# Performance work log

Hardware: AMD Instinct MI355X
Metric: run time of the kernel (lower is better)

The kernel has to match this reference:

```python
import jax, jax.numpy as jnp
import numpy as np

VOCAB = 100000
EMB_DIM = 64
NUM_DT_BUCKETS = 128
PAD_DT_ID = 0
B, L = 4096, 200


def setup_inputs() -> dict:
    key = jax.random.key(0)
    k1, k2, k3, k4, k5, k6 = jax.random.split(key, 6)
    items_pad = jax.random.randint(k1, (B, L), 0, VOCAB, dtype=jnp.int64 if jax.config.jax_enable_x64 else jnp.int32)
    dts_pad = jax.random.randint(k2, (B, L), 0, NUM_DT_BUCKETS, dtype=items_pad.dtype)
    mask = jax.random.randint(k3, (B, L), 0, 2) > 0
    mask = mask.at[:, 0].set(True)  # guarantee at least one valid position per row
    cand_items = jax.random.randint(k4, (B,), 0, VOCAB, dtype=items_pad.dtype)
    item_emb = jax.random.normal(k5, (VOCAB, EMB_DIM), dtype=jnp.float32) * 0.02
    dt_gate = jax.random.normal(k6, (NUM_DT_BUCKETS, 1), dtype=jnp.float32) * 0.02
    raw_tau = jnp.asarray(0.0, dtype=jnp.float32)
    return {
        "items_pad": items_pad,
        "dts_pad": dts_pad,
        "mask": mask,
        "cand_items": cand_items,
        "item_emb": item_emb,
        "dt_gate": dt_gate,
        "raw_tau": raw_tau,
    }


def reference(items_pad, dts_pad, mask, cand_items, item_emb, dt_gate, raw_tau):
    # padding_idx=0 on dt_gate: row PAD_DT_ID is zero
    dt_gate = dt_gate.at[PAD_DT_ID].set(0.0)
    k = item_emb[items_pad]                # [B, L, D]
    q = item_emb[cand_items]               # [B, D]
    sim = jnp.einsum('bld,bd->bl', k, q)   # [B, L]
    gate = dt_gate[dts_pad][..., 0]        # [B, L]
    tau = jax.nn.softplus(raw_tau) + 1e-6
    logits = sim * gate / tau
    logits = jnp.where(mask, logits, -jnp.inf)
    attn = jax.nn.softmax(logits, axis=1)  # [B, L]
    u = jnp.einsum('bl,bld->bd', attn, k)  # [B, D]
    return u, attn, tau
```

## Files before the change

### kernel.cpp

```cpp
#include <hip/hip_runtime.h>
#include <math.h>


constexpr int Bsz  = 4096;
constexpr int Lseq = 200;
constexpr int Dim  = 64;
constexpr int WPB  = 4;

__global__ __launch_bounds__(256, 2)
void cac_kernel(const int* __restrict__ items,
                const int* __restrict__ dts,
                const int* __restrict__ mask,
                const int* __restrict__ cand,
                const float* __restrict__ emb,
                const float* __restrict__ gate,
                const float* __restrict__ rawtau,
                float* __restrict__ out_u,
                float* __restrict__ out_attn,
                float* __restrict__ out_tau)
{
    __shared__ int   cpos[WPB][Lseq];
    __shared__ int   crow[WPB][Lseq];
    __shared__ float cgate[WPB][Lseq];
    __shared__ float clog[WPB][Lseq];

    const int tid  = threadIdx.x;
    const int wv   = tid >> 6;
    const int lane = tid & 63;
    const int b    = blockIdx.x * WPB + wv;

    const float raw = rawtau[0];
    const float sp  = (raw > 20.f) ? raw : log1pf(expf(raw));
    const float tau = sp + 1e-6f;
    const float inv_tau = 1.0f / tau;
    if (b == 0 && tid == 0) out_tau[0] = tau;

    int rowk[4], mk[4];
    float gk[4];
    #pragma unroll
    for (int k = 0; k < 4; ++k) {
        const int  p  = k * 64 + lane;
        const bool in = (p < Lseq);
        rowk[k] = in ? items[(size_t)b * Lseq + p] : 0;
        mk[k]   = in ? mask[(size_t)b * Lseq + p] : 0;
        const int dt = in ? dts[(size_t)b * Lseq + p] : 0;
        gk[k] = (dt == 0) ? 0.f : gate[dt];
    }

    unsigned long long bals[4];
    int offs[5];
    offs[0] = 0;
    #pragma unroll
    for (int k = 0; k < 4; ++k) {
        bals[k] = __ballot(mk[k] != 0);
        offs[k + 1] = offs[k] + __popcll(bals[k]);
    }
    const int cnt = offs[4];
    const unsigned long long ltmask = (1ull << lane) - 1ull;
    #pragma unroll
    for (int k = 0; k < 4; ++k) {
        if (mk[k]) {
            const int idx = offs[k] + __popcll(bals[k] & ltmask);
            cpos[wv][idx]  = k * 64 + lane;
            crow[wv][idx]  = rowk[k];
            cgate[wv][idx] = gk[k];
        }
    }

    const int r = lane >> 2;
    const int j = lane & 3;
    const float4* qrow = (const float4*)(emb + (size_t)cand[b] * Dim);
    float4 qv[4];
    #pragma unroll
    for (int i = 0; i < 4; ++i) qv[i] = qrow[i * 4 + j];

    float acc[16];
    #pragma unroll
    for (int i = 0; i < 16; ++i) acc[i] = 0.f;
    float m = -INFINITY, s_l = 0.f;

    const int ngrp = (cnt + 15) >> 4;
    for (int g = 0; g < ngrp; ++g) {
        const int  e     = g * 16 + r;
        const bool valid = (e < cnt);
        const int  ec    = valid ? e : (cnt - 1);
        const int  row   = crow[wv][ec];
        const float cg   = cgate[wv][ec];
        const float4* kp = (const float4*)(emb + (size_t)row * Dim);
        float4 kv[4];
        #pragma unroll
        for (int i = 0; i < 4; ++i) kv[i] = kp[i * 4 + j];

        float p = 0.f;
        #pragma unroll
        for (int i = 0; i < 4; ++i) {
            p = fmaf(kv[i].x, qv[i].x, p);
            p = fmaf(kv[i].y, qv[i].y, p);
            p = fmaf(kv[i].z, qv[i].z, p);
            p = fmaf(kv[i].w, qv[i].w, p);
        }
        p += __shfl_xor(p, 1, 64);
        p += __shfl_xor(p, 2, 64);

        const float logit = p * cg * inv_tau;
        const float leff  = valid ? logit : -INFINITY;

        float gm = leff;
        #pragma unroll
        for (int off = 4; off < 64; off <<= 1)
            gm = fmaxf(gm, __shfl_xor(gm, off, 64));

        if (gm > m) {
            const float scale = __expf(m - gm);
            s_l *= scale;
            #pragma unroll
            for (int i = 0; i < 16; ++i) acc[i] *= scale;
            m = gm;
        }

        const float wgt = __expf(leff - m);
        if (valid && j == 0) clog[wv][e] = logit;
        if (j == 0) s_l += wgt;
        #pragma unroll
        for (int i = 0; i < 4; ++i) {
            acc[4 * i + 0] = fmaf(wgt, kv[i].x, acc[4 * i + 0]);
            acc[4 * i + 1] = fmaf(wgt, kv[i].y, acc[4 * i + 1]);
            acc[4 * i + 2] = fmaf(wgt, kv[i].z, acc[4 * i + 2]);
            acc[4 * i + 3] = fmaf(wgt, kv[i].w, acc[4 * i + 3]);
        }
    }

    #pragma unroll
    for (int off = 4; off < 64; off <<= 1) {
        #pragma unroll
        for (int i = 0; i < 16; ++i) acc[i] += __shfl_xor(acc[i], off, 64);
    }
    float s = s_l;
    #pragma unroll
    for (int off = 1; off < 64; off <<= 1) s += __shfl_xor(s, off, 64);
    const float inv_s = 1.0f / s;

    if (r == 0) {
        float4* up = (float4*)(out_u + (size_t)b * Dim);
        #pragma unroll
        for (int i = 0; i < 4; ++i) {
            float4 o;
            o.x = acc[4 * i + 0] * inv_s;
            o.y = acc[4 * i + 1] * inv_s;
            o.z = acc[4 * i + 2] * inv_s;
            o.w = acc[4 * i + 3] * inv_s;
            up[i * 4 + j] = o;
        }
    }

    #pragma unroll
    for (int k = 0; k < 4; ++k) {
        const int p = k * 64 + lane;
        if (p < Lseq && !mk[k]) out_attn[(size_t)b * Lseq + p] = 0.f;
    }
    for (int e = lane; e < cnt; e += 64) {
        const float a = __expf(clog[wv][e] - m) * inv_s;
        out_attn[(size_t)b * Lseq + cpos[wv][e]] = a;
    }
}

extern "C" void kernel_launch(void* const* d_in, const int* in_sizes, int n_in,
                              void* d_out, int out_size, void* d_ws, size_t ws_size,
                              hipStream_t stream) {
    const int*   items  = (const int*)  d_in[0];
    const int*   dts    = (const int*)  d_in[1];
    const int*   mask   = (const int*)  d_in[2];
    const int*   cand   = (const int*)  d_in[3];
    const float* emb    = (const float*)d_in[4];
    const float* gate   = (const float*)d_in[5];
    const float* rawtau = (const float*)d_in[6];

    float* out_u    = (float*)d_out;
    float* out_attn = out_u + Bsz * Dim;
    float* out_tau  = out_attn + Bsz * Lseq;

    cac_kernel<<<Bsz / WPB, 256, 0, stream>>>(items, dts, mask, cand, emb, gate,
                                              rawtau, out_u, out_attn, out_tau);
}
```

Baseline: 100.8 us.

## Process two key rows per lane group and prefetch next group's embeddings

The online-softmax loop now handles 32 compacted positions per iteration, two per 4-lane group instead of one. It also software-prefetches the next iteration's embedding rows into registers before computing on the current ones. The aim is to raise memory-level parallelism on the random gather of embedding rows and to halve the number of cross-lane max reductions. In exchange register pressure roughly doubles for the key data (32 extra floats per lane), which could limit occupancy under the 256x2 launch bounds.

```diff
diff --git a/kernel.cpp b/kernel.cpp
--- a/kernel.cpp
+++ b/kernel.cpp
@@ -79,33 +79,61 @@
     for (int i = 0; i < 16; ++i) acc[i] = 0.f;
     float m = -INFINITY, s_l = 0.f;
 
-    const int ngrp = (cnt + 15) >> 4;
+    const int ngrp = (cnt + 31) >> 5;
+
+    int e0 = r, e1 = 16 + r;
+    int ec0 = (e0 < cnt) ? e0 : (cnt - 1);
+    int ec1 = (e1 < cnt) ? e1 : (cnt - 1);
+    int   row0 = crow[wv][ec0],  row1 = crow[wv][ec1];
+    float cg0  = cgate[wv][ec0], cg1  = cgate[wv][ec1];
+    float4 kv0[4], kv1[4];
+    {
+        const float4* kp0 = (const float4*)(emb + (size_t)row0 * Dim);
+        const float4* kp1 = (const float4*)(emb + (size_t)row1 * Dim);
+        #pragma unroll
+        for (int i = 0; i < 4; ++i) kv0[i] = kp0[i * 4 + j];
+        #pragma unroll
+        for (int i = 0; i < 4; ++i) kv1[i] = kp1[i * 4 + j];
+    }
+
     for (int g = 0; g < ngrp; ++g) {
-        const int  e     = g * 16 + r;
-        const bool valid = (e < cnt);
-        const int  ec    = valid ? e : (cnt - 1);
-        const int  row   = crow[wv][ec];
-        const float cg   = cgate[wv][ec];
-        const float4* kp = (const float4*)(emb + (size_t)row * Dim);
-        float4 kv[4];
-        #pragma unroll
-        for (int i = 0; i < 4; ++i) kv[i] = kp[i * 4 + j];
-
-        float p = 0.f;
+        const int gn = (g + 1 < ngrp) ? (g + 1) : g;
+        const int ne0 = gn * 32 + r, ne1 = ne0 + 16;
+        const int nec0 = (ne0 < cnt) ? ne0 : (cnt - 1);
+        const int nec1 = (ne1 < cnt) ? ne1 : (cnt - 1);
+        const int   nrow0 = crow[wv][nec0],  nrow1 = crow[wv][nec1];
+        const float ncg0  = cgate[wv][nec0], ncg1  = cgate[wv][nec1];
+        float4 nkv0[4], nkv1[4];
+        {
+            const float4* np0 = (const float4*)(emb + (size_t)nrow0 * Dim);
+            const float4* np1 = (const float4*)(emb + (size_t)nrow1 * Dim);
+            #pragma unroll
+            for (int i = 0; i < 4; ++i) nkv0[i] = np0[i * 4 + j];
+            #pragma unroll
+            for (int i = 0; i < 4; ++i) nkv1[i] = np1[i * 4 + j];
+        }
+
+        float p0 = 0.f, p1 = 0.f;
         #pragma unroll
         for (int i = 0; i < 4; ++i) {
-            p = fmaf(kv[i].x, qv[i].x, p);
-            p = fmaf(kv[i].y, qv[i].y, p);
-            p = fmaf(kv[i].z, qv[i].z, p);
-            p = fmaf(kv[i].w, qv[i].w, p);
-        }
-        p += __shfl_xor(p, 1, 64);
-        p += __shfl_xor(p, 2, 64);
-
-        const float logit = p * cg * inv_tau;
-        const float leff  = valid ? logit : -INFINITY;
-
-        float gm = leff;
+            p0 = fmaf(kv0[i].x, qv[i].x, p0);
+            p0 = fmaf(kv0[i].y, qv[i].y, p0);
+            p0 = fmaf(kv0[i].z, qv[i].z, p0);
+            p0 = fmaf(kv0[i].w, qv[i].w, p0);
+            p1 = fmaf(kv1[i].x, qv[i].x, p1);
+            p1 = fmaf(kv1[i].y, qv[i].y, p1);
+            p1 = fmaf(kv1[i].z, qv[i].z, p1);
+            p1 = fmaf(kv1[i].w, qv[i].w, p1);
+        }
+        p0 += __shfl_xor(p0, 1, 64);  p0 += __shfl_xor(p0, 2, 64);
+        p1 += __shfl_xor(p1, 1, 64);  p1 += __shfl_xor(p1, 2, 64);
+
+        const float logit0 = p0 * cg0 * inv_tau;
+        const float logit1 = p1 * cg1 * inv_tau;
+        const float leff0  = (e0 < cnt) ? logit0 : -INFINITY;
+        const float leff1  = (e1 < cnt) ? logit1 : -INFINITY;
+
+        float gm = fmaxf(leff0, leff1);
         #pragma unroll
         for (int off = 4; off < 64; off <<= 1)
             gm = fmaxf(gm, __shfl_xor(gm, off, 64));
@@ -118,16 +146,23 @@
             m = gm;
         }
 
-        const float wgt = __expf(leff - m);
-        if (valid && j == 0) clog[wv][e] = logit;
-        if (j == 0) s_l += wgt;
+        const float w0 = __expf(leff0 - m);
+        const float w1 = __expf(leff1 - m);
+        if (e0 < cnt && j == 0) clog[wv][e0] = logit0;
+        if (e1 < cnt && j == 0) clog[wv][e1] = logit1;
+        if (j == 0) s_l += w0 + w1;
         #pragma unroll
         for (int i = 0; i < 4; ++i) {
-            acc[4 * i + 0] = fmaf(wgt, kv[i].x, acc[4 * i + 0]);
-            acc[4 * i + 1] = fmaf(wgt, kv[i].y, acc[4 * i + 1]);
-            acc[4 * i + 2] = fmaf(wgt, kv[i].z, acc[4 * i + 2]);
-            acc[4 * i + 3] = fmaf(wgt, kv[i].w, acc[4 * i + 3]);
-        }
+            acc[4 * i + 0] = fmaf(w0, kv0[i].x, fmaf(w1, kv1[i].x, acc[4 * i + 0]));
+            acc[4 * i + 1] = fmaf(w0, kv0[i].y, fmaf(w1, kv1[i].y, acc[4 * i + 1]));
+            acc[4 * i + 2] = fmaf(w0, kv0[i].z, fmaf(w1, kv1[i].z, acc[4 * i + 2]));
+            acc[4 * i + 3] = fmaf(w0, kv0[i].w, fmaf(w1, kv1[i].w, acc[4 * i + 3]));
+        }
+
+        e0 = ne0; e1 = ne1;
+        cg0 = ncg0; cg1 = ncg1;
+        #pragma unroll
+        for (int i = 0; i < 4; ++i) { kv0[i] = nkv0[i]; kv1[i] = nkv1[i]; }
     }
 
     #pragma unroll
```

Result: no change. 102.6 us (+1.8%).

## Split each row across two wavefronts with shared-memory softmax merge

Applied to the files above, without the earlier changes.

Each batch row is now processed by two wavefronts instead of one. Each wavefront covers half of the compacted valid positions, and the partial max, sum and weighted accumulators are merged through shared memory. This halves the serial gather/online-softmax chain per wave and doubles the block count to improve latency hiding. It adds two block barriers and leaves the second wave idle during the compaction phase.

```diff
diff --git a/kernel.cpp b/kernel.cpp
--- a/kernel.cpp
+++ b/kernel.cpp
@@ -5,9 +5,9 @@
 constexpr int Bsz  = 4096;
 constexpr int Lseq = 200;
 constexpr int Dim  = 64;
-constexpr int WPB  = 4;
-
-__global__ __launch_bounds__(256, 2)
+constexpr int RPB  = 2;
+
+__global__ __launch_bounds__(256, 4)
 void cac_kernel(const int* __restrict__ items,
                 const int* __restrict__ dts,
                 const int* __restrict__ mask,
@@ -19,53 +19,27 @@
                 float* __restrict__ out_attn,
                 float* __restrict__ out_tau)
 {
-    __shared__ int   cpos[WPB][Lseq];
-    __shared__ int   crow[WPB][Lseq];
-    __shared__ float cgate[WPB][Lseq];
-    __shared__ float clog[WPB][Lseq];
+    __shared__ int   cpos[RPB][Lseq];
+    __shared__ int   crow[RPB][Lseq];
+    __shared__ float cgate[RPB][Lseq];
+    __shared__ float clog[RPB][Lseq];
+    __shared__ int   cnt_lds[RPB];
+    __shared__ float pu[RPB][2][Dim];
+    __shared__ float pm[RPB][2];
+    __shared__ float ps[RPB][2];
 
     const int tid  = threadIdx.x;
     const int wv   = tid >> 6;
     const int lane = tid & 63;
-    const int b    = blockIdx.x * WPB + wv;
+    const int slot = wv >> 1;
+    const int half = wv & 1;
+    const int b    = blockIdx.x * RPB + slot;
 
     const float raw = rawtau[0];
     const float sp  = (raw > 20.f) ? raw : log1pf(expf(raw));
     const float tau = sp + 1e-6f;
     const float inv_tau = 1.0f / tau;
-    if (b == 0 && tid == 0) out_tau[0] = tau;
-
-    int rowk[4], mk[4];
-    float gk[4];
-    #pragma unroll
-    for (int k = 0; k < 4; ++k) {
-        const int  p  = k * 64 + lane;
-        const bool in = (p < Lseq);
-        rowk[k] = in ? items[(size_t)b * Lseq + p] : 0;
-        mk[k]   = in ? mask[(size_t)b * Lseq + p] : 0;
-        const int dt = in ? dts[(size_t)b * Lseq + p] : 0;
-        gk[k] = (dt == 0) ? 0.f : gate[dt];
-    }
-
-    unsigned long long bals[4];
-    int offs[5];
-    offs[0] = 0;
-    #pragma unroll
-    for (int k = 0; k < 4; ++k) {
-        bals[k] = __ballot(mk[k] != 0);
-        offs[k + 1] = offs[k] + __popcll(bals[k]);
-    }
-    const int cnt = offs[4];
-    const unsigned long long ltmask = (1ull << lane) - 1ull;
-    #pragma unroll
-    for (int k = 0; k < 4; ++k) {
-        if (mk[k]) {
-            const int idx = offs[k] + __popcll(bals[k] & ltmask);
-            cpos[wv][idx]  = k * 64 + lane;
-            crow[wv][idx]  = rowk[k];
-            cgate[wv][idx] = gk[k];
-        }
-    }
+    if (blockIdx.x == 0 && tid == 0) out_tau[0] = tau;
 
     const int r = lane >> 2;
     const int j = lane & 3;
@@ -74,18 +48,63 @@
     #pragma unroll
     for (int i = 0; i < 4; ++i) qv[i] = qrow[i * 4 + j];
 
+    int mz[2];
+    #pragma unroll
+    for (int k = 0; k < 2; ++k) {
+        const int p = (2 * half + k) * 64 + lane;
+        mz[k] = (p < Lseq) ? mask[(size_t)b * Lseq + p] : 1;
+    }
+
+    if (half == 0) {
+        int rowk[4], mk[4];
+        float gk[4];
+        #pragma unroll
+        for (int k = 0; k < 4; ++k) {
+            const int  p  = k * 64 + lane;
+            const bool in = (p < Lseq);
+            rowk[k] = in ? items[(size_t)b * Lseq + p] : 0;
+            mk[k]   = in ? mask[(size_t)b * Lseq + p] : 0;
+            const int dt = in ? dts[(size_t)b * Lseq + p] : 0;
+            gk[k] = (dt == 0) ? 0.f : gate[dt];
+        }
+        unsigned long long bals[4];
+        int offs[5];
+        offs[0] = 0;
+        #pragma unroll
+        for (int k = 0; k < 4; ++k) {
+            bals[k] = __ballot(mk[k] != 0);
+            offs[k + 1] = offs[k] + __popcll(bals[k]);
+        }
+        const unsigned long long ltmask = (1ull << lane) - 1ull;
+        #pragma unroll
+        for (int k = 0; k < 4; ++k) {
+            if (mk[k]) {
+                const int idx = offs[k] + __popcll(bals[k] & ltmask);
+                cpos[slot][idx]  = k * 64 + lane;
+                crow[slot][idx]  = rowk[k];
+                cgate[slot][idx] = gk[k];
+            }
+        }
+        if (lane == 0) cnt_lds[slot] = offs[4];
+    }
+    __syncthreads();
+
+    const int cnt = cnt_lds[slot];
+    const int h   = (cnt + 1) >> 1;
+    const int elo = half ? h : 0;
+    const int ehi = half ? cnt : h;
+
     float acc[16];
     #pragma unroll
     for (int i = 0; i < 16; ++i) acc[i] = 0.f;
     float m = -INFINITY, s_l = 0.f;
 
-    const int ngrp = (cnt + 15) >> 4;
-    for (int g = 0; g < ngrp; ++g) {
-        const int  e     = g * 16 + r;
-        const bool valid = (e < cnt);
-        const int  ec    = valid ? e : (cnt - 1);
-        const int  row   = crow[wv][ec];
-        const float cg   = cgate[wv][ec];
+    for (int g = elo; g < ehi; g += 16) {
+        const int  e     = g + r;
+        const bool valid = (e < ehi);
+        const int  ec    = valid ? e : (ehi - 1);
+        const int  row   = crow[slot][ec];
+        const float cg   = cgate[slot][ec];
         const float4* kp = (const float4*)(emb + (size_t)row * Dim);
         float4 kv[4];
         #pragma unroll
@@ -119,7 +138,7 @@
         }
 
         const float wgt = __expf(leff - m);
-        if (valid && j == 0) clog[wv][e] = logit;
+        if (valid && j == 0) clog[slot][e] = logit;
         if (j == 0) s_l += wgt;
         #pragma unroll
         for (int i = 0; i < 4; ++i) {
@@ -138,29 +157,37 @@
     float s = s_l;
     #pragma unroll
     for (int off = 1; off < 64; off <<= 1) s += __shfl_xor(s, off, 64);
-    const float inv_s = 1.0f / s;
 
     if (r == 0) {
-        float4* up = (float4*)(out_u + (size_t)b * Dim);
         #pragma unroll
         for (int i = 0; i < 4; ++i) {
             float4 o;
-            o.x = acc[4 * i + 0] * inv_s;
-            o.y = acc[4 * i + 1] * inv_s;
-            o.z = acc[4 * i + 2] * inv_s;
-            o.w = acc[4 * i + 3] * inv_s;
-            up[i * 4 + j] = o;
-        }
-    }
-
-    #pragma unroll
-    for (int k = 0; k < 4; ++k) {
-        const int p = k * 64 + lane;
-        if (p < Lseq && !mk[k]) out_attn[(size_t)b * Lseq + p] = 0.f;
-    }
-    for (int e = lane; e < cnt; e += 64) {
-        const float a = __expf(clog[wv][e] - m) * inv_s;
-        out_attn[(size_t)b * Lseq + cpos[wv][e]] = a;
+            o.x = acc[4 * i + 0]; o.y = acc[4 * i + 1];
+            o.z = acc[4 * i + 2]; o.w = acc[4 * i + 3];
+            *(float4*)&pu[slot][half][i * 16 + 4 * j] = o;
+        }
+    }
+    if (lane == 0) { pm[slot][half] = m; ps[slot][half] = s; }
+    __syncthreads();
+
+    const float mA = pm[slot][0], mB = pm[slot][1];
+    const float mf = fmaxf(mA, mB);
+    const float cA = __expf(mA - mf), cB = __expf(mB - mf);
+    const float sf = ps[slot][0] * cA + ps[slot][1] * cB;
+    const float inv_sf = 1.0f / sf;
+
+    if (half == 0)
+        out_u[(size_t)b * Dim + lane] =
+            (pu[slot][0][lane] * cA + pu[slot][1][lane] * cB) * inv_sf;
+
+    #pragma unroll
+    for (int k = 0; k < 2; ++k) {
+        const int p = (2 * half + k) * 64 + lane;
+        if (p < Lseq && !mz[k]) out_attn[(size_t)b * Lseq + p] = 0.f;
+    }
+    for (int e = elo + lane; e < ehi; e += 64) {
+        const float a = __expf(clog[slot][e] - mf) * inv_sf;
+        out_attn[(size_t)b * Lseq + cpos[slot][e]] = a;
     }
 }
 
@@ -179,6 +206,6 @@
     float* out_attn = out_u + Bsz * Dim;
     float* out_tau  = out_attn + Bsz * Lseq;
 
-    cac_kernel<<<Bsz / WPB, 256, 0, stream>>>(items, dts, mask, cand, emb, gate,
+    cac_kernel<<<Bsz / RPB, 256, 0, stream>>>(items, dts, mask, cand, emb, gate,
                                               rawtau, out_u, out_attn, out_tau);
 }
```

After: 105.0 us. 4.2% more time.
